# Optimization experiments

Hardware: AMD Instinct MI355X
Metric: run time of the kernel (lower is better)

## Reference

```python
import jax, jax.numpy as jnp
import numpy as np

NUM_HEADS = 12
ATTN_BALANCE = 0.3
ROPE_THETA = 10000.0
EPS = 1e-4


def _mp_weight(w):
    # Eval-mode MPConv weight prep: per-output-channel magnitude-preserving
    # normalize (normalize() with alpha=sqrt(1/fan_in)), then scale by gain/sqrt(fan_in).
    O = w.shape[0]
    fan = int(np.prod(w.shape[1:]))  # in_channels * 1 * 1
    wf = w.astype(jnp.float32).reshape(O, -1)
    n = jnp.linalg.norm(wf, axis=1, keepdims=True)
    wn = wf / (EPS + n / np.sqrt(fan))
    return wn / np.sqrt(fan)  # [O, fan]; 1x1 kernel -> acts as a dense matrix


def _normalize_lastdim(x):
    # normalize(y, dim=-1): denom = eps + ||x||_2 * sqrt(1/c)
    c = x.shape[-1]
    n = jnp.linalg.norm(x.astype(jnp.float32), axis=-1, keepdims=True)
    return x / (EPS + n / np.sqrt(c)).astype(x.dtype)


def _rope(q, k):
    c = q.shape[-1]
    t = q.shape[2]
    inv_freq = 1.0 / (ROPE_THETA ** (jnp.arange(0, c, 2, dtype=jnp.float32) / c))  # [c/2]
    ang = jnp.arange(t, dtype=jnp.float32)[:, None] * inv_freq                      # [t, c/2]
    cos = jnp.cos(ang)[None, None, :, None, :]
    sin = jnp.sin(ang)[None, None, :, None, :]

    def rot(x):
        x1, x2 = jnp.split(x, 2, axis=-1)
        return jnp.concatenate([x1 * cos - x2 * sin, x2 * cos + x1 * sin], axis=-1)

    return rot(q), rot(k)


def setup_inputs() -> dict:
    key = jax.random.key(0)
    k1, k2, k3 = jax.random.split(key, 3)
    B, C, H, W = 32, 768, 16, 16  # B = batch_size * n_frames = 2 * 16
    x = jax.random.normal(k1, (B, C, H, W), dtype=jnp.float32)
    w_qkv = jax.random.normal(k2, (3 * C, C, 1, 1), dtype=jnp.float32)
    w_proj = jax.random.normal(k3, (C, C, 1, 1), dtype=jnp.float32)
    return {"x": x, "w_qkv": w_qkv, "w_proj": w_proj, "batch_size": 2}


def reference(x, w_qkv, w_proj, batch_size):
    B, C, H, W = x.shape
    m = NUM_HEADS
    c = C // m
    t = B // batch_size
    i = H * W
    T = t * i

    wq = _mp_weight(w_qkv).astype(x.dtype)   # [3C, C]
    wp = _mp_weight(w_proj).astype(x.dtype)  # [C, C]

    # 1x1 conv == channel matmul
    y = jnp.einsum('bchw,oc->bohw', x, wq)
    # '(b t) (s m c) h w -> b s m t (h w) c'
    y = y.reshape(batch_size, t, 3, m, c, i).transpose(0, 2, 3, 1, 5, 4)  # [b,3,m,t,i,c]
    y = _normalize_lastdim(y)
    q, k, v = y[:, 0], y[:, 1], y[:, 2]  # each [b, m, t, i, c]
    q, k = _rope(q, k)

    q = q.reshape(batch_size, m, T, c)
    k = k.reshape(batch_size, m, T, c)
    v = v.reshape(batch_size, m, T, c)

    # frame-causal block mask: q_frame >= kv_frame (infer-mode mask of the module)
    scores = jnp.einsum('bmqc,bmkc->bmqk', q, k) / np.sqrt(c)
    frame = jnp.arange(T) // i
    mask = frame[:, None] >= frame[None, :]  # [T, T] bool, block structure over frames
    scores = jnp.where(mask, scores, -jnp.inf)
    attn = jax.nn.softmax(scores, axis=-1)
    o = jnp.einsum('bmqk,bmkc->bmqc', attn, v)

    # 'b m (t h w) c -> (b t) (c m) h w'  (channel index = c_idx * m + m_idx)
    o = o.reshape(batch_size, m, t, H, W, c).transpose(0, 2, 5, 1, 3, 4).reshape(B, C, H, W)
    o = jnp.einsum('bchw,oc->bohw', o, wp)

    tt = ATTN_BALANCE  # mp_sum(x, o, t)
    return (x + tt * (o - x)) / np.sqrt((1.0 - tt) ** 2 + tt ** 2)
```

## Files before the change

### kernel.cpp

```cpp
#include <hip/hip_runtime.h>
#include <hip/hip_bf16.h>
#include <math.h>

typedef __hip_bfloat16 bf16;
typedef __attribute__((ext_vector_type(8))) short short8;
typedef __attribute__((ext_vector_type(4))) float f32x4;

#define EPSV 0.0001f

__device__ __forceinline__ unsigned short f2bf(float f) {
    unsigned int u = __float_as_uint(f);
    u += 0x7fff + ((u >> 16) & 1);
    return (unsigned short)(u >> 16);
}

__global__ __launch_bounds__(256) void rownorm_cast_kernel(
    const float* __restrict__ w_qkv, const float* __restrict__ w_proj,
    unsigned short* __restrict__ Wqb, unsigned short* __restrict__ Wpb)
{
    const int row = blockIdx.x;
    const float* src;
    unsigned short* dst;
    if (row < 2304) { src = w_qkv + (size_t)row * 768;           dst = Wqb + (size_t)row * 768; }
    else            { src = w_proj + (size_t)(row - 2304) * 768; dst = Wpb + (size_t)(row - 2304) * 768; }

    const int tid = threadIdx.x;
    float v[3];
    float ss = 0.f;
    #pragma unroll
    for (int j = 0; j < 3; j++) {
        v[j] = src[tid + j * 256];
        ss += v[j] * v[j];
    }
    #pragma unroll
    for (int off = 32; off > 0; off >>= 1) ss += __shfl_down(ss, off, 64);
    __shared__ float wsum[4];
    if ((tid & 63) == 0) wsum[tid >> 6] = ss;
    __syncthreads();
    const float total = wsum[0] + wsum[1] + wsum[2] + wsum[3];
    const float scale = 1.0f / (EPSV * 27.712812921102035f + sqrtf(total));
    #pragma unroll
    for (int j = 0; j < 3; j++) dst[tid + j * 256] = f2bf(v[j] * scale);
}

__global__ __launch_bounds__(256) void cast_x_kernel(
    const float* __restrict__ X, unsigned short* __restrict__ XbT)
{
    const int c0 = blockIdx.x * 64;
    const int b  = blockIdx.y;
    const int pos = threadIdx.x;
    const float* src = X + ((size_t)b * 768 + c0) * 256 + pos;
    unsigned short* dst = XbT + ((size_t)b * 256 + pos) * 768 + c0;
    #pragma unroll
    for (int cc = 0; cc < 8; cc++) {
        short8 t;
        #pragma unroll
        for (int j = 0; j < 8; j++)
            t[j] = (short)f2bf(src[(size_t)(cc * 8 + j) * 256]);
        *(short8*)&dst[cc * 8] = t;
    }
}

__global__ __launch_bounds__(256, 2) void qkv_mfma_kernel(
    const unsigned short* __restrict__ Wqb,
    const unsigned short* __restrict__ XbT,
    bf16* __restrict__ Q, bf16* __restrict__ K, bf16* __restrict__ Vt)
{
    const int g = blockIdx.x;
    const int b = blockIdx.y;
    const int bs = b >> 4, fr = b & 15;
    const int qkv = g / 12, head = g % 12;
    const int m0 = g * 64;

    const int tid = threadIdx.x;
    const int w = tid >> 6, lane = tid & 63;
    const int l15 = lane & 15, quad = lane >> 4;

    __shared__ unsigned short As[64 * 72];
    __shared__ unsigned short Bs[256 * 72];

    const unsigned short* Ag = Wqb + (size_t)m0 * 768;
    const unsigned short* Bg = XbT + (size_t)b * 256 * 768;

    f32x4 acc[4][4];
    #pragma unroll
    for (int mi = 0; mi < 4; mi++)
        #pragma unroll
        for (int ni = 0; ni < 4; ni++)
            acc[mi][ni] = (f32x4){0.f, 0.f, 0.f, 0.f};

    const int arow = tid >> 2, acol = (tid & 3) * 16;
    const int brow = tid >> 3, bcol = (tid & 7) * 8;

    for (int k0 = 0; k0 < 768; k0 += 64) {
        const short8 av0 = *(const short8*)&Ag[(size_t)arow * 768 + k0 + acol];
        const short8 av1 = *(const short8*)&Ag[(size_t)arow * 768 + k0 + acol + 8];
        short8 bv[8];
        #pragma unroll
        for (int p = 0; p < 8; p++)
            bv[p] = *(const short8*)&Bg[(size_t)(32 * p + brow) * 768 + k0 + bcol];
        __syncthreads();
        *(short8*)&As[arow * 72 + acol] = av0;
        *(short8*)&As[arow * 72 + acol + 8] = av1;
        #pragma unroll
        for (int p = 0; p < 8; p++)
            *(short8*)&Bs[(32 * p + brow) * 72 + bcol] = bv[p];
        __syncthreads();

        short8 af[4][2], bfr[4][2];
        #pragma unroll
        for (int mi = 0; mi < 4; mi++)
            #pragma unroll
            for (int kk = 0; kk < 2; kk++)
                af[mi][kk] = *(const short8*)&As[(16 * mi + l15) * 72 + 32 * kk + 8 * quad];
        #pragma unroll
        for (int ni = 0; ni < 4; ni++)
            #pragma unroll
            for (int kk = 0; kk < 2; kk++)
                bfr[ni][kk] = *(const short8*)&Bs[(64 * w + 16 * ni + l15) * 72 + 32 * kk + 8 * quad];
        #pragma unroll
        for (int kk = 0; kk < 2; kk++)
            #pragma unroll
            for (int mi = 0; mi < 4; mi++)
                #pragma unroll
                for (int ni = 0; ni < 4; ni++)
                    acc[mi][ni] = __builtin_amdgcn_mfma_f32_16x16x32_bf16(af[mi][kk], bfr[ni][kk], acc[mi][ni], 0, 0, 0);
    }

    float inv[4];
    #pragma unroll
    for (int ni = 0; ni < 4; ni++) {
        float ssq = 0.f;
        #pragma unroll
        for (int mi = 0; mi < 4; mi++)
            #pragma unroll
            for (int r = 0; r < 4; r++)
                ssq = fmaf(acc[mi][ni][r], acc[mi][ni][r], ssq);
        ssq += __shfl_xor(ssq, 16, 64);
        ssq += __shfl_xor(ssq, 32, 64);
        inv[ni] = 1.0f / (EPSV + sqrtf(ssq) * 0.125f);
    }

    if (qkv == 2) {
        unsigned short* Vb = &Bs[w * 64 * 72];
        #pragma unroll
        for (int ni = 0; ni < 4; ni++)
            #pragma unroll
            for (int mi = 0; mi < 4; mi++) {
                uint2 d;
                d.x = (unsigned int)f2bf(acc[mi][ni][0] * inv[ni]) |
                      ((unsigned int)f2bf(acc[mi][ni][1] * inv[ni]) << 16);
                d.y = (unsigned int)f2bf(acc[mi][ni][2] * inv[ni]) |
                      ((unsigned int)f2bf(acc[mi][ni][3] * inv[ni]) << 16);
                *(uint2*)&Vb[(16 * ni + l15) * 72 + 16 * mi + 4 * quad] = d;
            }
        unsigned short* Vtu = (unsigned short*)Vt;
        const size_t cb = ((size_t)(bs * 12 + head) * 64);
        const int tok = fr * 256 + 64 * w + lane;
        #pragma unroll 8
        for (int ch = 0; ch < 64; ch++)
            Vtu[(cb + ch) * 4096 + tok] = Vb[lane * 72 + ch];
    } else {
        unsigned short* dst = (unsigned short*)((qkv == 0) ? Q : K);
        const float post = (qkv == 0) ? 0.125f : 1.0f;
        #pragma unroll
        for (int ni = 0; ni < 4; ni++) {
            const int token = fr * 256 + 64 * w + 16 * ni + l15;
            const size_t base = (((size_t)(bs * 12 + head)) * 4096 + token) * 64;
            #pragma unroll
            for (int mi = 0; mi < 2; mi++) {
                unsigned int lo[2], hi[2];
                #pragma unroll
                for (int r = 0; r < 4; r++) {
                    const int j = 16 * mi + 4 * quad + r;
                    const float n1 = acc[mi][ni][r] * inv[ni];
                    const float n2 = acc[mi + 2][ni][r] * inv[ni];
                    const float ang = (float)fr * exp2f(-(float)j * 0.41524101186092029f);
                    float sn, cs;
                    __sincosf(ang, &sn, &cs);
                    const unsigned short o1 = f2bf((n1 * cs - n2 * sn) * post);
                    const unsigned short o2 = f2bf((n2 * cs + n1 * sn) * post);
                    if (r < 2) { if (r == 0) { lo[0] = o1; hi[0] = o2; } else { lo[0] |= (unsigned int)o1 << 16; hi[0] |= (unsigned int)o2 << 16; } }
                    else       { if (r == 2) { lo[1] = o1; hi[1] = o2; } else { lo[1] |= (unsigned int)o1 << 16; hi[1] |= (unsigned int)o2 << 16; } }
                }
                *(uint2*)&dst[base + 16 * mi + 4 * quad]      = make_uint2(lo[0], lo[1]);
                *(uint2*)&dst[base + 32 + 16 * mi + 4 * quad] = make_uint2(hi[0], hi[1]);
            }
        }
    }
}

__global__ __launch_bounds__(256, 4) void attn_mfma_kernel(
    const bf16* __restrict__ Qg, const bf16* __restrict__ Kg,
    const bf16* __restrict__ Vtg, unsigned short* __restrict__ OspT)
{
    const int qtile = 63 - blockIdx.x;
    const int qfr = qtile >> 2;
    const int head = blockIdx.y, bs = blockIdx.z;
    const int tid = threadIdx.x;
    const int w = tid >> 6, lane = tid & 63;
    const int l15 = lane & 15, quad = lane >> 4;
    const size_t hb = ((size_t)(bs * 12 + head)) * 4096 * 64;

    __shared__ unsigned short Ks[64 * 72];
    __shared__ unsigned short Vs[64 * 72];
    __shared__ unsigned short Pw[4][16 * 40];

    const unsigned short* Qu = (const unsigned short*)Qg;
    const unsigned short* Ku = (const unsigned short*)Kg;
    const unsigned short* Vu = (const unsigned short*)Vtg;

    short8 Qf[2];
    {
        const int qrow = qfr * 256 + (qtile & 3) * 64 + w * 16 + l15;
        #pragma unroll
        for (int kk = 0; kk < 2; kk++)
            Qf[kk] = *(const short8*)&Qu[hb + (size_t)qrow * 64 + 32 * kk + 8 * quad];
    }

    f32x4 O[4];
    #pragma unroll
    for (int c = 0; c < 4; c++) O[c] = (f32x4){0.f, 0.f, 0.f, 0.f};
    float lsum = 0.f;
    const f32x4 zf = (f32x4){0.f, 0.f, 0.f, 0.f};

    const int stage_row = tid >> 2;
    const int stage_off = (tid & 3) * 16;
    const unsigned short* Kst = Ku + hb + stage_off;
    const unsigned short* Vst = Vu + hb + (size_t)stage_row * 4096 + stage_off;

    short8 ka = *(const short8*)&Kst[(size_t)stage_row * 64];
    short8 kb = *(const short8*)&Kst[(size_t)stage_row * 64 + 8];
    short8 va = *(const short8*)&Vst[0];
    short8 vb = *(const short8*)&Vst[8];

    const int nk = (qfr + 1) * 256;
    for (int t0 = 0; t0 < nk; t0 += 64) {
        __syncthreads();
        *(short8*)&Ks[stage_row * 72 + stage_off] = ka;
        *(short8*)&Ks[stage_row * 72 + stage_off + 8] = kb;
        *(short8*)&Vs[stage_row * 72 + stage_off] = va;
        *(short8*)&Vs[stage_row * 72 + stage_off + 8] = vb;
        __syncthreads();

        const int tn = (t0 + 64 < nk) ? t0 + 64 : t0;
        ka = *(const short8*)&Kst[(size_t)(tn + stage_row) * 64];
        kb = *(const short8*)&Kst[(size_t)(tn + stage_row) * 64 + 8];
        va = *(const short8*)&Vst[tn];
        vb = *(const short8*)&Vst[tn + 8];

        f32x4 St[4];
        #pragma unroll
        for (int mi = 0; mi < 4; mi++) {
            const short8 kf0 = *(const short8*)&Ks[(16 * mi + l15) * 72 + 8 * quad];
            const short8 kf1 = *(const short8*)&Ks[(16 * mi + l15) * 72 + 32 + 8 * quad];
            f32x4 s = __builtin_amdgcn_mfma_f32_16x16x32_bf16(kf0, Qf[0], zf, 0, 0, 0);
            St[mi] = __builtin_amdgcn_mfma_f32_16x16x32_bf16(kf1, Qf[1], s, 0, 0, 0);
        }

        #pragma unroll
        for (int mi = 0; mi < 4; mi++) {
            const f32x4 s = St[mi];
            const float p0 = __expf(s[0] - 8.f);
            const float p1 = __expf(s[1] - 8.f);
            const float p2 = __expf(s[2] - 8.f);
            const float p3 = __expf(s[3] - 8.f);
            lsum += (p0 + p1) + (p2 + p3);
            uint2 d;
            d.x = (unsigned int)f2bf(p0) | ((unsigned int)f2bf(p1) << 16);
            d.y = (unsigned int)f2bf(p2) | ((unsigned int)f2bf(p3) << 16);
            *(uint2*)&Pw[w][l15 * 40 + 16 * mi + 4 * quad] = d;
        }

        short8 Pf[2];
        #pragma unroll
        for (int ks = 0; ks < 2; ks++)
            Pf[ks] = *(const short8*)&Pw[w][l15 * 40 + 32 * ks + 8 * quad];

        #pragma unroll
        for (int ci = 0; ci < 4; ci++) {
            const short8 vf0 = *(const short8*)&Vs[(16 * ci + l15) * 72 + 8 * quad];
            const short8 vf1 = *(const short8*)&Vs[(16 * ci + l15) * 72 + 32 + 8 * quad];
            O[ci] = __builtin_amdgcn_mfma_f32_16x16x32_bf16(Pf[0], vf0, O[ci], 0, 0, 0);
            O[ci] = __builtin_amdgcn_mfma_f32_16x16x32_bf16(Pf[1], vf1, O[ci], 0, 0, 0);
        }
    }

    lsum += __shfl_xor(lsum, 16, 64);
    lsum += __shfl_xor(lsum, 32, 64);
    lsum = 1.0f / lsum;

    const size_t ob = ((size_t)(bs * 16 + qfr)) * 196608;
    #pragma unroll
    for (int r = 0; r < 4; r++) {
        const float inv = __shfl(lsum, quad * 4 + r, 64);
        const int pos = (qtile & 3) * 64 + w * 16 + 4 * quad + r;
        #pragma unroll
        for (int ci = 0; ci < 4; ci++) {
            const int chan = (16 * ci + l15) * 12 + head;
            OspT[ob + (size_t)pos * 768 + chan] = f2bf(O[ci][r] * inv);
        }
    }
}

__global__ __launch_bounds__(256, 2) void proj_mfma_kernel(
    const unsigned short* __restrict__ Wpb,
    const unsigned short* __restrict__ OspT,
    const float* __restrict__ X,
    float* __restrict__ Out)
{
    const int my = blockIdx.x;
    const int b  = blockIdx.y;
    const int m0 = my * 64;

    const int tid = threadIdx.x;
    const int w = tid >> 6, lane = tid & 63;
    const int l15 = lane & 15, quad = lane >> 4;

    __shared__ unsigned short As[64 * 72];
    __shared__ unsigned short Bs[256 * 72];

    const unsigned short* Ag = Wpb + (size_t)m0 * 768;
    const unsigned short* Bg = OspT + (size_t)b * 256 * 768;

    f32x4 acc[4][4];
    #pragma unroll
    for (int mi = 0; mi < 4; mi++)
        #pragma unroll
        for (int ni = 0; ni < 4; ni++)
            acc[mi][ni] = (f32x4){0.f, 0.f, 0.f, 0.f};

    const int arow = tid >> 2, acol = (tid & 3) * 16;
    const int brow = tid >> 3, bcol = (tid & 7) * 8;

    for (int k0 = 0; k0 < 768; k0 += 64) {
        const short8 av0 = *(const short8*)&Ag[(size_t)arow * 768 + k0 + acol];
        const short8 av1 = *(const short8*)&Ag[(size_t)arow * 768 + k0 + acol + 8];
        short8 bv[8];
        #pragma unroll
        for (int p = 0; p < 8; p++)
            bv[p] = *(const short8*)&Bg[(size_t)(32 * p + brow) * 768 + k0 + bcol];
        __syncthreads();
        *(short8*)&As[arow * 72 + acol] = av0;
        *(short8*)&As[arow * 72 + acol + 8] = av1;
        #pragma unroll
        for (int p = 0; p < 8; p++)
            *(short8*)&Bs[(32 * p + brow) * 72 + bcol] = bv[p];
        __syncthreads();

        short8 af[4][2], bfr[4][2];
        #pragma unroll
        for (int mi = 0; mi < 4; mi++)
            #pragma unroll
            for (int kk = 0; kk < 2; kk++)
                af[mi][kk] = *(const short8*)&As[(16 * mi + l15) * 72 + 32 * kk + 8 * quad];
        #pragma unroll
        for (int ni = 0; ni < 4; ni++)
            #pragma unroll
            for (int kk = 0; kk < 2; kk++)
                bfr[ni][kk] = *(const short8*)&Bs[(64 * w + 16 * ni + l15) * 72 + 32 * kk + 8 * quad];
        #pragma unroll
        for (int kk = 0; kk < 2; kk++)
            #pragma unroll
            for (int mi = 0; mi < 4; mi++)
                #pragma unroll
                for (int ni = 0; ni < 4; ni++)
                    acc[mi][ni] = __builtin_amdgcn_mfma_f32_16x16x32_bf16(af[mi][kk], bfr[ni][kk], acc[mi][ni], 0, 0, 0);
    }

    const float kMix = 1.3130643285972254f;
    #pragma unroll
    for (int mi = 0; mi < 4; mi++)
        #pragma unroll
        for (int r = 0; r < 4; r++) {
            const int m = m0 + 16 * mi + 4 * quad + r;
            const size_t rowb = (size_t)b * 196608 + (size_t)m * 256;
            #pragma unroll
            for (int ni = 0; ni < 4; ni++) {
                const int n = 64 * w + 16 * ni + l15;
                Out[rowb + n] = (0.7f * X[rowb + n] + 0.3f * acc[mi][ni][r]) * kMix;
            }
        }
}

extern "C" void kernel_launch(void* const* d_in, const int* in_sizes, int n_in,
                              void* d_out, int out_size, void* d_ws, size_t ws_size,
                              hipStream_t stream) {
    const float* x     = (const float*)d_in[0];
    const float* wqkv  = (const float*)d_in[1];
    const float* wproj = (const float*)d_in[2];
    float* out = (float*)d_out;

    char* ws = (char*)d_ws;
    unsigned short* Wqb  = (unsigned short*)(ws + 0);
    unsigned short* Wpb  = (unsigned short*)(ws + 3538944);
    unsigned short* XbT  = (unsigned short*)(ws + 4718592);
    unsigned short* OspT = XbT;
    bf16*  Q   = (bf16*)(ws + 17301504);
    bf16*  K   = (bf16*)(ws + 29884416);
    bf16*  Vt  = (bf16*)(ws + 42467328);

    rownorm_cast_kernel<<<3072, 256, 0, stream>>>(wqkv, wproj, Wqb, Wpb);
    cast_x_kernel<<<dim3(12, 32), 256, 0, stream>>>(x, XbT);
    qkv_mfma_kernel<<<dim3(36, 32), 256, 0, stream>>>(Wqb, XbT, Q, K, Vt);
    attn_mfma_kernel<<<dim3(64, 12, 2), 256, 0, stream>>>(Q, K, Vt, OspT);
    proj_mfma_kernel<<<dim3(12, 32), 256, 0, stream>>>(Wpb, OspT, x, out);
}
```

Measured before the change: 307.7 us.

## Pair complementary causal query frames per attention block to balance work and reuse K/V

Each attention block now handles two query tiles, one from frame p and one from frame 15-p. Every block therefore walks the same total number of key tiles, and each staged K/V tile in shared memory feeds both query sets. The goal is to remove the load imbalance of the frame-causal mask and halve the K/V staging traffic per query. It also switches exp to a native exp2 with a folded log2e constant and uses packed hardware bf16 conversion. In exchange, registers grow from the doubled accumulators, so launch bounds drop from 4 to 3 blocks per CU, and the grid halves.

```diff
diff --git a/kernel.cpp b/kernel.cpp
--- a/kernel.cpp
+++ b/kernel.cpp
@@ -12,6 +12,13 @@
     unsigned int u = __float_as_uint(f);
     u += 0x7fff + ((u >> 16) & 1);
     return (unsigned short)(u >> 16);
+}
+__device__ __forceinline__ unsigned int pkbf(float a, float b) {
+    __hip_bfloat162 h = __float22bfloat162_rn(make_float2(a, b));
+    return *(unsigned int*)&h;
+}
+__device__ __forceinline__ float fast_exp2(float x) {
+    return __builtin_amdgcn_exp2f(x);
 }
 
 __global__ __launch_bounds__(256) void rownorm_cast_kernel(
@@ -148,10 +155,8 @@
             #pragma unroll
             for (int mi = 0; mi < 4; mi++) {
                 uint2 d;
-                d.x = (unsigned int)f2bf(acc[mi][ni][0] * inv[ni]) |
-                      ((unsigned int)f2bf(acc[mi][ni][1] * inv[ni]) << 16);
-                d.y = (unsigned int)f2bf(acc[mi][ni][2] * inv[ni]) |
-                      ((unsigned int)f2bf(acc[mi][ni][3] * inv[ni]) << 16);
+                d.x = pkbf(acc[mi][ni][0] * inv[ni], acc[mi][ni][1] * inv[ni]);
+                d.y = pkbf(acc[mi][ni][2] * inv[ni], acc[mi][ni][3] * inv[ni]);
                 *(uint2*)&Vb[(16 * ni + l15) * 72 + 16 * mi + 4 * quad] = d;
             }
         unsigned short* Vtu = (unsigned short*)Vt;
@@ -190,12 +195,13 @@
     }
 }
 
-__global__ __launch_bounds__(256, 4) void attn_mfma_kernel(
+__global__ __launch_bounds__(256, 3) void attn_mfma_kernel(
     const bf16* __restrict__ Qg, const bf16* __restrict__ Kg,
     const bf16* __restrict__ Vtg, unsigned short* __restrict__ OspT)
 {
-    const int qtile = 63 - blockIdx.x;
-    const int qfr = qtile >> 2;
+    const int px = blockIdx.x;
+    const int p = px >> 2, sub = px & 3;
+    const int fa = p, fb = 15 - p;
     const int head = blockIdx.y, bs = blockIdx.z;
     const int tid = threadIdx.x;
     const int w = tid >> 6, lane = tid & 63;
@@ -204,25 +210,33 @@
 
     __shared__ unsigned short Ks[64 * 72];
     __shared__ unsigned short Vs[64 * 72];
-    __shared__ unsigned short Pw[4][16 * 40];
+    __shared__ unsigned short Pw[4][2][16 * 72];
 
     const unsigned short* Qu = (const unsigned short*)Qg;
     const unsigned short* Ku = (const unsigned short*)Kg;
     const unsigned short* Vu = (const unsigned short*)Vtg;
 
-    short8 Qf[2];
+    short8 Qfa[2], Qfb[2];
     {
-        const int qrow = qfr * 256 + (qtile & 3) * 64 + w * 16 + l15;
-        #pragma unroll
-        for (int kk = 0; kk < 2; kk++)
-            Qf[kk] = *(const short8*)&Qu[hb + (size_t)qrow * 64 + 32 * kk + 8 * quad];
-    }
-
-    f32x4 O[4];
-    #pragma unroll
-    for (int c = 0; c < 4; c++) O[c] = (f32x4){0.f, 0.f, 0.f, 0.f};
-    float lsum = 0.f;
+        const int qra = fa * 256 + sub * 64 + w * 16 + l15;
+        const int qrb = fb * 256 + sub * 64 + w * 16 + l15;
+        #pragma unroll
+        for (int kk = 0; kk < 2; kk++) {
+            Qfa[kk] = *(const short8*)&Qu[hb + (size_t)qra * 64 + 32 * kk + 8 * quad];
+            Qfb[kk] = *(const short8*)&Qu[hb + (size_t)qrb * 64 + 32 * kk + 8 * quad];
+        }
+    }
+
+    f32x4 Oa[4], Ob[4];
+    #pragma unroll
+    for (int c = 0; c < 4; c++) {
+        Oa[c] = (f32x4){0.f, 0.f, 0.f, 0.f};
+        Ob[c] = (f32x4){0.f, 0.f, 0.f, 0.f};
+    }
+    float la = 0.f, lb = 0.f;
     const f32x4 zf = (f32x4){0.f, 0.f, 0.f, 0.f};
+    const float L2E = 1.4426950408889634f;
+    const float C = 11.541560327111707f;
 
     const int stage_row = tid >> 2;
     const int stage_off = (tid & 3) * 16;
@@ -234,8 +248,9 @@
     short8 va = *(const short8*)&Vst[0];
     short8 vb = *(const short8*)&Vst[8];
 
-    const int nk = (qfr + 1) * 256;
-    for (int t0 = 0; t0 < nk; t0 += 64) {
+    const int nka = (fa + 1) * 256;
+    const int nkb = (fb + 1) * 256;
+    for (int t0 = 0; t0 < nkb; t0 += 64) {
         __syncthreads();
         *(short8*)&Ks[stage_row * 72 + stage_off] = ka;
         *(short8*)&Ks[stage_row * 72 + stage_off + 8] = kb;
@@ -243,62 +258,98 @@
         *(short8*)&Vs[stage_row * 72 + stage_off + 8] = vb;
         __syncthreads();
 
-        const int tn = (t0 + 64 < nk) ? t0 + 64 : t0;
+        const int tn = (t0 + 64 < nkb) ? t0 + 64 : t0;
         ka = *(const short8*)&Kst[(size_t)(tn + stage_row) * 64];
         kb = *(const short8*)&Kst[(size_t)(tn + stage_row) * 64 + 8];
         va = *(const short8*)&Vst[tn];
         vb = *(const short8*)&Vst[tn + 8];
 
-        f32x4 St[4];
+        const bool doA = (t0 < nka);
+
+        f32x4 Sa[4], Sb[4];
         #pragma unroll
         for (int mi = 0; mi < 4; mi++) {
             const short8 kf0 = *(const short8*)&Ks[(16 * mi + l15) * 72 + 8 * quad];
             const short8 kf1 = *(const short8*)&Ks[(16 * mi + l15) * 72 + 32 + 8 * quad];
-            f32x4 s = __builtin_amdgcn_mfma_f32_16x16x32_bf16(kf0, Qf[0], zf, 0, 0, 0);
-            St[mi] = __builtin_amdgcn_mfma_f32_16x16x32_bf16(kf1, Qf[1], s, 0, 0, 0);
+            f32x4 s = __builtin_amdgcn_mfma_f32_16x16x32_bf16(kf0, Qfb[0], zf, 0, 0, 0);
+            Sb[mi] = __builtin_amdgcn_mfma_f32_16x16x32_bf16(kf1, Qfb[1], s, 0, 0, 0);
+            if (doA) {
+                f32x4 sa = __builtin_amdgcn_mfma_f32_16x16x32_bf16(kf0, Qfa[0], zf, 0, 0, 0);
+                Sa[mi] = __builtin_amdgcn_mfma_f32_16x16x32_bf16(kf1, Qfa[1], sa, 0, 0, 0);
+            }
         }
 
         #pragma unroll
         for (int mi = 0; mi < 4; mi++) {
-            const f32x4 s = St[mi];
-            const float p0 = __expf(s[0] - 8.f);
-            const float p1 = __expf(s[1] - 8.f);
-            const float p2 = __expf(s[2] - 8.f);
-            const float p3 = __expf(s[3] - 8.f);
-            lsum += (p0 + p1) + (p2 + p3);
+            const f32x4 s = Sb[mi];
+            const float p0 = fast_exp2(fmaf(s[0], L2E, -C));
+            const float p1 = fast_exp2(fmaf(s[1], L2E, -C));
+            const float p2 = fast_exp2(fmaf(s[2], L2E, -C));
+            const float p3 = fast_exp2(fmaf(s[3], L2E, -C));
+            lb += (p0 + p1) + (p2 + p3);
             uint2 d;
-            d.x = (unsigned int)f2bf(p0) | ((unsigned int)f2bf(p1) << 16);
-            d.y = (unsigned int)f2bf(p2) | ((unsigned int)f2bf(p3) << 16);
-            *(uint2*)&Pw[w][l15 * 40 + 16 * mi + 4 * quad] = d;
-        }
-
-        short8 Pf[2];
+            d.x = pkbf(p0, p1);
+            d.y = pkbf(p2, p3);
+            *(uint2*)&Pw[w][1][l15 * 72 + 16 * mi + 4 * quad] = d;
+        }
+        if (doA) {
+            #pragma unroll
+            for (int mi = 0; mi < 4; mi++) {
+                const f32x4 s = Sa[mi];
+                const float p0 = fast_exp2(fmaf(s[0], L2E, -C));
+                const float p1 = fast_exp2(fmaf(s[1], L2E, -C));
+                const float p2 = fast_exp2(fmaf(s[2], L2E, -C));
+                const float p3 = fast_exp2(fmaf(s[3], L2E, -C));
+                la += (p0 + p1) + (p2 + p3);
+                uint2 d;
+                d.x = pkbf(p0, p1);
+                d.y = pkbf(p2, p3);
+                *(uint2*)&Pw[w][0][l15 * 72 + 16 * mi + 4 * quad] = d;
+            }
+        }
+
+        short8 Pfb[2], Pfa[2];
         #pragma unroll
         for (int ks = 0; ks < 2; ks++)
-            Pf[ks] = *(const short8*)&Pw[w][l15 * 40 + 32 * ks + 8 * quad];
+            Pfb[ks] = *(const short8*)&Pw[w][1][l15 * 72 + 32 * ks + 8 * quad];
+        if (doA) {
+            #pragma unroll
+            for (int ks = 0; ks < 2; ks++)
+                Pfa[ks] = *(const short8*)&Pw[w][0][l15 * 72 + 32 * ks + 8 * quad];
+        }
 
         #pragma unroll
         for (int ci = 0; ci < 4; ci++) {
             const short8 vf0 = *(const short8*)&Vs[(16 * ci + l15) * 72 + 8 * quad];
             const short8 vf1 = *(const short8*)&Vs[(16 * ci + l15) * 72 + 32 + 8 * quad];
-            O[ci] = __builtin_amdgcn_mfma_f32_16x16x32_bf16(Pf[0], vf0, O[ci], 0, 0, 0);
-            O[ci] = __builtin_amdgcn_mfma_f32_16x16x32_bf16(Pf[1], vf1, O[ci], 0, 0, 0);
-        }
-    }
-
-    lsum += __shfl_xor(lsum, 16, 64);
-    lsum += __shfl_xor(lsum, 32, 64);
-    lsum = 1.0f / lsum;
-
-    const size_t ob = ((size_t)(bs * 16 + qfr)) * 196608;
+            Ob[ci] = __builtin_amdgcn_mfma_f32_16x16x32_bf16(Pfb[0], vf0, Ob[ci], 0, 0, 0);
+            Ob[ci] = __builtin_amdgcn_mfma_f32_16x16x32_bf16(Pfb[1], vf1, Ob[ci], 0, 0, 0);
+            if (doA) {
+                Oa[ci] = __builtin_amdgcn_mfma_f32_16x16x32_bf16(Pfa[0], vf0, Oa[ci], 0, 0, 0);
+                Oa[ci] = __builtin_amdgcn_mfma_f32_16x16x32_bf16(Pfa[1], vf1, Oa[ci], 0, 0, 0);
+            }
+        }
+    }
+
+    la += __shfl_xor(la, 16, 64);
+    la += __shfl_xor(la, 32, 64);
+    la = 1.0f / la;
+    lb += __shfl_xor(lb, 16, 64);
+    lb += __shfl_xor(lb, 32, 64);
+    lb = 1.0f / lb;
+
+    const size_t oba = ((size_t)(bs * 16 + fa)) * 196608;
+    const size_t obb = ((size_t)(bs * 16 + fb)) * 196608;
     #pragma unroll
     for (int r = 0; r < 4; r++) {
-        const float inv = __shfl(lsum, quad * 4 + r, 64);
-        const int pos = (qtile & 3) * 64 + w * 16 + 4 * quad + r;
+        const float ia = __shfl(la, quad * 4 + r, 64);
+        const float ib = __shfl(lb, quad * 4 + r, 64);
+        const int pos = sub * 64 + w * 16 + 4 * quad + r;
         #pragma unroll
         for (int ci = 0; ci < 4; ci++) {
             const int chan = (16 * ci + l15) * 12 + head;
-            OspT[ob + (size_t)pos * 768 + chan] = f2bf(O[ci][r] * inv);
+            OspT[oba + (size_t)pos * 768 + chan] = f2bf(Oa[ci][r] * ia);
+            OspT[obb + (size_t)pos * 768 + chan] = f2bf(Ob[ci][r] * ib);
         }
     }
 }
@@ -403,6 +454,6 @@
     rownorm_cast_kernel<<<3072, 256, 0, stream>>>(wqkv, wproj, Wqb, Wpb);
     cast_x_kernel<<<dim3(12, 32), 256, 0, stream>>>(x, XbT);
     qkv_mfma_kernel<<<dim3(36, 32), 256, 0, stream>>>(Wqb, XbT, Q, K, Vt);
-    attn_mfma_kernel<<<dim3(64, 12, 2), 256, 0, stream>>>(Q, K, Vt, OspT);
+    attn_mfma_kernel<<<dim3(32, 12, 2), 256, 0, stream>>>(Q, K, Vt, OspT);
     proj_mfma_kernel<<<dim3(12, 32), 256, 0, stream>>>(Wpb, OspT, x, out);
 }
```

Result: faster. 261.3 us (-15.1%).
